# Kernel optimization log

Measured on AMD Instinct MI355X. Metric: run time of the kernel, lower is better.

The kernel has to match this reference:

```python
import jax, jax.numpy as jnp
import numpy as np

B, N, P, E = 4, 512, 2048, 32768  # batch, atoms/sample, probes/sample, edges/sample
F_HID = 128
D_RBF = 32
CUTOFF = 4.0
CELL_L = 10.0


def setup_inputs() -> dict:
    key = jax.random.key(0)
    ks = jax.random.split(key, 12)
    in_dim = D_RBF + 3 * F_HID
    inp = {
        "S_JK": jax.random.normal(ks[0], (B * N, F_HID), jnp.float32),
        "V_JK": jax.random.normal(ks[1], (B * N, 3, F_HID), jnp.float32) * 0.5,
        "atom_xyz": jax.random.uniform(ks[2], (B, N, 3), jnp.float32) * CELL_L,
        "probe_xyz": jax.random.uniform(ks[3], (B, P, 3), jnp.float32) * CELL_L,
        "cell": jnp.tile(CELL_L * jnp.eye(3, dtype=jnp.float32), (B, 1, 1)),
        "probe_edges_displacement": jax.random.randint(ks[4], (B, E, 3), -1, 2).astype(jnp.float32),
        "W1": jax.random.normal(ks[5], (in_dim, F_HID), jnp.float32) / np.sqrt(in_dim),
        "b1": jnp.zeros((F_HID,), jnp.float32),
        "W2": jax.random.normal(ks[6], (F_HID, F_HID // 2), jnp.float32) / np.sqrt(F_HID),
        "b2": jnp.zeros((F_HID // 2,), jnp.float32),
        "W3": jax.random.normal(ks[7], (F_HID // 2, 1), jnp.float32) / np.sqrt(F_HID // 2),
        "b3": jnp.zeros((1,), jnp.float32),
        "probe_edges": jnp.stack([
            jax.random.randint(ks[8], (B, E), 0, N),
            jax.random.randint(ks[9], (B, E), 0, P),
        ], axis=-1),
    }
    return inp


def reference(S_JK, V_JK, atom_xyz, probe_xyz, cell, probe_edges_displacement,
              W1, b1, W2, b2, W3, b3, probe_edges):
    # full counts -> unpad_and_cat == reshape
    atom_flat = atom_xyz.reshape(B * N, 3)
    probe_flat = probe_xyz.reshape(B * P, 3)
    a_idx = (probe_edges[..., 0] + (jnp.arange(B) * N)[:, None]).reshape(-1)  # [B*E]
    p_idx = (probe_edges[..., 1] + (jnp.arange(B) * P)[:, None]).reshape(-1)

    # periodic displacement: edges_displacement @ cell (per batch), then flatten
    disp = jnp.einsum('bek,bkj->bej', probe_edges_displacement, cell).reshape(-1, 3)
    diff = probe_flat[p_idx] - (atom_flat[a_idx] + disp)          # [BE,3]
    dist = jnp.linalg.norm(diff, axis=-1)                         # [BE]

    # sinc RBF expansion: sin(n*pi*d/cutoff)/d, n=1..D_RBF
    n_range = jnp.arange(1, D_RBF + 1, dtype=dist.dtype)
    e_pi = jnp.sin(dist[:, None] * n_range * jnp.pi / CUTOFF) / dist[:, None]

    r_hat = diff / (dist[:, None] + 1e-8)                          # [BE,3]
    q_pi = jnp.einsum('ekf,ek->ef', V_JK[a_idx], r_hat)            # [BE,F]
    n_e = jnp.linalg.norm(V_JK, axis=1)[a_idx]                     # [BE,F]

    h = jnp.concatenate([e_pi, q_pi, n_e, S_JK[a_idx]], axis=-1)   # [BE, D_RBF+3F]
    h = jax.nn.silu(h @ W1 + b1)
    h = jax.nn.silu(h @ W2 + b2)
    m_pi = (h @ W3 + b3)[:, 0]                                     # [BE]

    # Behler-Parinello cosine cutoff
    cw = jnp.where(dist < CUTOFF, 0.5 * (jnp.cos(jnp.pi * dist / CUTOFF) + 1.0), 0.0)
    m_weighted = m_pi * cw

    rho = jax.ops.segment_sum(m_weighted, p_idx, num_segments=B * P)
    return rho.reshape(B, P)
```

## Files before the change

### kernel.cpp

```cpp
#include <hip/hip_runtime.h>
#include <math.h>

#define BB 4
#define NN 512
#define PP 2048
#define EE 32768
#define FH 128
#define DRBF 32
#define CUT 4.0f
#define PI_F 3.14159265358979323846f
#define NE 4
#define CHUNK 256
#define AT2 8


__global__ __launch_bounds__(256) void atom_kernel(
    const float* __restrict__ S, const float* __restrict__ V,
    const float* __restrict__ W1, float* __restrict__ O,
    float* __restrict__ out) {
  __shared__ float inS[AT2][128];
  const int t   = threadIdx.x;
  if (blockIdx.x < 8)
    ((float4*)out)[blockIdx.x * 256 + t] = make_float4(0.f, 0.f, 0.f, 0.f);

  const int fam = blockIdx.x % 5;
  const int a0  = (blockIdx.x / 5) * AT2;

  {
    int a  = t >> 5;
    int k4 = t & 31;
    float4 v;
    if (fam < 3) {
      v = *(const float4*)&V[(size_t)(a0 + a) * 384 + fam * 128 + k4 * 4];
    } else if (fam == 4) {
      v = *(const float4*)&S[(size_t)(a0 + a) * 128 + k4 * 4];
    } else {
      float4 x = *(const float4*)&V[(size_t)(a0 + a) * 384 +   0 + k4 * 4];
      float4 y = *(const float4*)&V[(size_t)(a0 + a) * 384 + 128 + k4 * 4];
      float4 z = *(const float4*)&V[(size_t)(a0 + a) * 384 + 256 + k4 * 4];
      v.x = sqrtf(x.x*x.x + y.x*y.x + z.x*z.x);
      v.y = sqrtf(x.y*x.y + y.y*y.y + z.y*z.y);
      v.z = sqrtf(x.z*x.z + y.z*y.z + z.z*z.z);
      v.w = sqrtf(x.w*x.w + y.w*y.w + z.w*z.w);
    }
    *(float4*)&inS[a][k4 * 4] = v;
  }
  __syncthreads();

  const int f1 = t & 127;
  const int ah = t >> 7;
  const int wrow = (fam < 3) ? 32 : ((fam == 3) ? 160 : 288);
  const float* Wb = W1 + (size_t)wrow * FH + f1;

  float acc0 = 0.f, acc1 = 0.f, acc2 = 0.f, acc3 = 0.f;
  #pragma unroll 4
  for (int k4 = 0; k4 < 32; ++k4) {
    float w0 = Wb[(k4*4 + 0) * FH];
    float w1 = Wb[(k4*4 + 1) * FH];
    float w2 = Wb[(k4*4 + 2) * FH];
    float w3 = Wb[(k4*4 + 3) * FH];
    float4 h0 = *(const float4*)&inS[ah*4 + 0][k4*4];
    float4 h1 = *(const float4*)&inS[ah*4 + 1][k4*4];
    float4 h2 = *(const float4*)&inS[ah*4 + 2][k4*4];
    float4 h3 = *(const float4*)&inS[ah*4 + 3][k4*4];
    acc0 = fmaf(h0.x, w0, acc0); acc1 = fmaf(h1.x, w0, acc1);
    acc2 = fmaf(h2.x, w0, acc2); acc3 = fmaf(h3.x, w0, acc3);
    acc0 = fmaf(h0.y, w1, acc0); acc1 = fmaf(h1.y, w1, acc1);
    acc2 = fmaf(h2.y, w1, acc2); acc3 = fmaf(h3.y, w1, acc3);
    acc0 = fmaf(h0.z, w2, acc0); acc1 = fmaf(h1.z, w2, acc1);
    acc2 = fmaf(h2.z, w2, acc2); acc3 = fmaf(h3.z, w2, acc3);
    acc0 = fmaf(h0.w, w3, acc0); acc1 = fmaf(h1.w, w3, acc1);
    acc2 = fmaf(h2.w, w3, acc2); acc3 = fmaf(h3.w, w3, acc3);
  }
  float* Ob = O + (size_t)(a0 + ah*4) * 640 + fam * 128 + f1;
  Ob[0]    = acc0;
  Ob[640]  = acc1;
  Ob[1280] = acc2;
  Ob[1920] = acc3;
}

__global__ __launch_bounds__(256) void fused_kernel(
    const int* __restrict__ pe, const float* __restrict__ pdisp,
    const float* __restrict__ cell, const float* __restrict__ atom_xyz,
    const float* __restrict__ probe_xyz,
    const float* __restrict__ O,
    const float* __restrict__ W1, const float* __restrict__ b1,
    const float* __restrict__ W2, const float* __restrict__ b2,
    const float* __restrict__ W3, const float* __restrict__ b3,
    float* __restrict__ out) {
  __shared__ float sdx[CHUNK], sdy[CHUNK], sdz[CHUNK];
  __shared__ unsigned sap[CHUNK];
  __shared__ int mcnt;
  __shared__ float epS[NE][DRBF];
  __shared__ float h2S[NE][FH];
  __shared__ float part2[4][NE][64];
  __shared__ float rS[NE][3];
  __shared__ unsigned aS[NE];
  __shared__ float cwS[NE];
  __shared__ unsigned pS[NE];

  const int t    = threadIdx.x;
  const int lane = t & 63;
  const int wave = t >> 6;
  if (t == 0) mcnt = 0;
  __syncthreads();

  const int e = blockIdx.x * CHUNK + t;
  const int b = blockIdx.x >> 7;
  const float* cb = cell + b * 9;
  {
    int2 ap = ((const int2*)pe)[e];
    float pd0 = pdisp[e*3], pd1 = pdisp[e*3+1], pd2 = pdisp[e*3+2];
    float d0 = pd0*cb[0] + pd1*cb[3] + pd2*cb[6];
    float d1 = pd0*cb[1] + pd1*cb[4] + pd2*cb[7];
    float d2 = pd0*cb[2] + pd1*cb[5] + pd2*cb[8];
    int ag = b*NN + ap.x;
    int pg = b*PP + ap.y;
    float dx = probe_xyz[pg*3]   - (atom_xyz[ag*3]   + d0);
    float dy = probe_xyz[pg*3+1] - (atom_xyz[ag*3+1] + d1);
    float dz = probe_xyz[pg*3+2] - (atom_xyz[ag*3+2] + d2);
    float dist2 = dx*dx + dy*dy + dz*dz;
    if (dist2 < CUT*CUT) {
      int s = atomicAdd(&mcnt, 1);
      sdx[s] = dx; sdy[s] = dy; sdz[s] = dz;
      sap[s] = ((unsigned)ag << 16) | (unsigned)pg;
    }
  }
  __syncthreads();
  const int m = mcnt;
  if (m == 0) return;

  const int f1 = t & 127;
  const int eh = t >> 7;
  const float b1v = b1[f1];
  const float b2v = b2[lane];
  const float w3v = W3[lane];
  const float b3v = b3[0];

  for (int s0 = 0; s0 < m; s0 += NE) {
    {
      const int s = s0 + wave;
      float dx, dy, dz; unsigned ap_;
      if (s < m) { dx = sdx[s]; dy = sdy[s]; dz = sdz[s]; ap_ = sap[s]; }
      else       { dx = 1.f; dy = 0.f; dz = 0.f; ap_ = 0xFFFFFFFFu; }
      float d = sqrtf(dx*dx + dy*dy + dz*dz);
      float inv = 1.0f / (d + 1e-8f);
      if (lane < DRBF) epS[wave][lane] = sinf(d * (float)(lane+1) * (PI_F/CUT)) / d;
      if (lane == 0) {
        rS[wave][0] = dx*inv; rS[wave][1] = dy*inv; rS[wave][2] = dz*inv;
        aS[wave] = (ap_ == 0xFFFFFFFFu) ? 0u : (ap_ >> 16);
        cwS[wave] = 0.5f * (cosf((PI_F/CUT) * d) + 1.0f);
        pS[wave]  = (ap_ == 0xFFFFFFFFu) ? 0xFFFFFFFFu : (ap_ & 0xFFFFu);
      }
    }
    __syncthreads();

    {
      const int e0 = eh*2, e1 = eh*2 + 1;
      const float* Ob0 = O + (size_t)aS[e0] * 640 + f1;
      const float* Ob1 = O + (size_t)aS[e1] * 640 + f1;
      float o00 = Ob0[0], o01 = Ob0[128], o02 = Ob0[256], o03 = Ob0[384], o04 = Ob0[512];
      float o10 = Ob1[0], o11 = Ob1[128], o12 = Ob1[256], o13 = Ob1[384], o14 = Ob1[512];
      float z0 = b1v + o03 + o04 + rS[e0][0]*o00 + rS[e0][1]*o01 + rS[e0][2]*o02;
      float z1 = b1v + o13 + o14 + rS[e1][0]*o10 + rS[e1][1]*o11 + rS[e1][2]*o12;
      const float* Wb = W1 + f1;
      #pragma unroll
      for (int k = 0; k < DRBF; ++k) {
        float w = Wb[k * FH];
        z0 = fmaf(epS[e0][k], w, z0);
        z1 = fmaf(epS[e1][k], w, z1);
      }
      h2S[e0][f1] = z0 / (1.0f + __expf(-z0));
      h2S[e1][f1] = z1 / (1.0f + __expf(-z1));
    }
    __syncthreads();

    {
      float a0 = 0.f, a1 = 0.f, a2 = 0.f, a3 = 0.f;
      const float* Wq = W2 + (wave * 32) * 64 + lane;
      const float* h0p = &h2S[0][wave * 32];
      const float* h1p = &h2S[1][wave * 32];
      const float* h2p = &h2S[2][wave * 32];
      const float* h3p = &h2S[3][wave * 32];
      #pragma unroll
      for (int k4 = 0; k4 < 8; ++k4) {
        float w0 = Wq[(k4*4 + 0) * 64];
        float w1 = Wq[(k4*4 + 1) * 64];
        float w2 = Wq[(k4*4 + 2) * 64];
        float w3 = Wq[(k4*4 + 3) * 64];
        float4 h0 = *(const float4*)&h0p[k4*4];
        float4 h1 = *(const float4*)&h1p[k4*4];
        float4 h2 = *(const float4*)&h2p[k4*4];
        float4 h3 = *(const float4*)&h3p[k4*4];
        a0 = fmaf(h0.x, w0, a0); a1 = fmaf(h1.x, w0, a1);
        a2 = fmaf(h2.x, w0, a2); a3 = fmaf(h3.x, w0, a3);
        a0 = fmaf(h0.y, w1, a0); a1 = fmaf(h1.y, w1, a1);
        a2 = fmaf(h2.y, w1, a2); a3 = fmaf(h3.y, w1, a3);
        a0 = fmaf(h0.z, w2, a0); a1 = fmaf(h1.z, w2, a1);
        a2 = fmaf(h2.z, w2, a2); a3 = fmaf(h3.z, w2, a3);
        a0 = fmaf(h0.w, w3, a0); a1 = fmaf(h1.w, w3, a1);
        a2 = fmaf(h2.w, w3, a2); a3 = fmaf(h3.w, w3, a3);
      }
      part2[wave][0][lane] = a0;
      part2[wave][1][lane] = a1;
      part2[wave][2][lane] = a2;
      part2[wave][3][lane] = a3;
    }
    __syncthreads();

    {
      float z = part2[0][wave][lane] + part2[1][wave][lane]
              + part2[2][wave][lane] + part2[3][wave][lane] + b2v;
      float h2 = z / (1.0f + __expf(-z));
      float rs = h2 * w3v;
      #pragma unroll
      for (int off = 32; off; off >>= 1) rs += __shfl_xor(rs, off, 64);
      if (lane == 0) {
        unsigned p = pS[wave];
        if (p != 0xFFFFFFFFu) atomicAdd(&out[p], (rs + b3v) * cwS[wave]);
      }
    }
    __syncthreads();
  }
}

extern "C" void kernel_launch(void* const* d_in, const int* in_sizes, int n_in,
                              void* d_out, int out_size, void* d_ws, size_t ws_size,
                              hipStream_t stream) {
  const float* S         = (const float*)d_in[0];
  const float* V         = (const float*)d_in[1];
  const float* atom_xyz  = (const float*)d_in[2];
  const float* probe_xyz = (const float*)d_in[3];
  const float* cell      = (const float*)d_in[4];
  const float* pdisp     = (const float*)d_in[5];
  const float* W1        = (const float*)d_in[6];
  const float* b1        = (const float*)d_in[7];
  const float* W2        = (const float*)d_in[8];
  const float* b2        = (const float*)d_in[9];
  const float* W3        = (const float*)d_in[10];
  const float* b3        = (const float*)d_in[11];
  const int*   pe        = (const int*)d_in[12];
  float* out = (float*)d_out;

  float* O = (float*)((char*)d_ws + 256);

  atom_kernel<<<(BB*NN/AT2)*5, 256, 0, stream>>>(S, V, W1, O, out);
  fused_kernel<<<BB*EE/CHUNK, 256, 0, stream>>>(pe, pdisp, cell, atom_xyz, probe_xyz,
                                                O, W1, b1, W2, b2, W3, b3, out);
}
```

Measured before the change: 22.30 us.

## Move edge filtering into atom kernel and compact survivors globally for MLP

Edge distance filtering now runs in extra blocks of the first kernel, alongside the per-atom projection. Surviving edges are appended to a global record buffer through an atomic counter. The MLP kernel then walks the compacted records in groups of four edges per block instead of re-filtering its own 256-edge chunk. This takes the gather and filter latency off the MLP kernel's critical path and balances work across blocks. In exchange it adds a memset launch and global atomics, and it silently drops survivors beyond a fixed cap of 8192 records.

```diff
diff --git a/kernel.cpp b/kernel.cpp
--- a/kernel.cpp
+++ b/kernel.cpp
@@ -10,21 +10,58 @@
 #define CUT 4.0f
 #define PI_F 3.14159265358979323846f
 #define NE 4
-#define CHUNK 256
 #define AT2 8
-
-
-__global__ __launch_bounds__(256) void atom_kernel(
+#define ABLK 1280
+#define FBLK 512
+#define RECMAX 8192
+
+struct __align__(16) Rec { float dx, dy, dz; unsigned ap; };
+
+
+__global__ __launch_bounds__(256) void combined_kernel(
+    const int* __restrict__ pe, const float* __restrict__ pdisp,
+    const float* __restrict__ cell, const float* __restrict__ atom_xyz,
+    const float* __restrict__ probe_xyz,
     const float* __restrict__ S, const float* __restrict__ V,
-    const float* __restrict__ W1, float* __restrict__ O,
-    float* __restrict__ out) {
+    const float* __restrict__ W1,
+    unsigned* __restrict__ gcnt, Rec* __restrict__ recs,
+    float* __restrict__ O, float* __restrict__ out) {
   __shared__ float inS[AT2][128];
   const int t   = threadIdx.x;
-  if (blockIdx.x < 8)
-    ((float4*)out)[blockIdx.x * 256 + t] = make_float4(0.f, 0.f, 0.f, 0.f);
-
-  const int fam = blockIdx.x % 5;
-  const int a0  = (blockIdx.x / 5) * AT2;
+  const int bid = blockIdx.x;
+
+  if (bid >= ABLK) {
+    const int fb = bid - ABLK;
+    const int e  = fb * 256 + t;
+    const int b  = e >> 15;
+    const float* cb = cell + b * 9;
+    int2 ap = ((const int2*)pe)[e];
+    float pd0 = pdisp[e*3], pd1 = pdisp[e*3+1], pd2 = pdisp[e*3+2];
+    float d0 = pd0*cb[0] + pd1*cb[3] + pd2*cb[6];
+    float d1 = pd0*cb[1] + pd1*cb[4] + pd2*cb[7];
+    float d2 = pd0*cb[2] + pd1*cb[5] + pd2*cb[8];
+    int ag = b*NN + ap.x;
+    int pg = b*PP + ap.y;
+    float dx = probe_xyz[pg*3]   - (atom_xyz[ag*3]   + d0);
+    float dy = probe_xyz[pg*3+1] - (atom_xyz[ag*3+1] + d1);
+    float dz = probe_xyz[pg*3+2] - (atom_xyz[ag*3+2] + d2);
+    float dist2 = dx*dx + dy*dy + dz*dz;
+    if (dist2 < CUT*CUT) {
+      unsigned i = atomicAdd(gcnt, 1u);
+      if (i < RECMAX) {
+        Rec r; r.dx = dx; r.dy = dy; r.dz = dz;
+        r.ap = ((unsigned)ag << 16) | (unsigned)pg;
+        recs[i] = r;
+      }
+    }
+    return;
+  }
+
+  if (bid < 8)
+    ((float4*)out)[bid * 256 + t] = make_float4(0.f, 0.f, 0.f, 0.f);
+
+  const int fam = bid % 5;
+  const int a0  = (bid / 5) * AT2;
 
   {
     int a  = t >> 5;
@@ -79,18 +116,13 @@
   Ob[1920] = acc3;
 }
 
-__global__ __launch_bounds__(256) void fused_kernel(
-    const int* __restrict__ pe, const float* __restrict__ pdisp,
-    const float* __restrict__ cell, const float* __restrict__ atom_xyz,
-    const float* __restrict__ probe_xyz,
+__global__ __launch_bounds__(256) void mlp_kernel(
+    const Rec* __restrict__ recs, const unsigned* __restrict__ gcnt,
     const float* __restrict__ O,
     const float* __restrict__ W1, const float* __restrict__ b1,
     const float* __restrict__ W2, const float* __restrict__ b2,
     const float* __restrict__ W3, const float* __restrict__ b3,
     float* __restrict__ out) {
-  __shared__ float sdx[CHUNK], sdy[CHUNK], sdz[CHUNK];
-  __shared__ unsigned sap[CHUNK];
-  __shared__ int mcnt;
   __shared__ float epS[NE][DRBF];
   __shared__ float h2S[NE][FH];
   __shared__ float part2[4][NE][64];
@@ -102,33 +134,8 @@
   const int t    = threadIdx.x;
   const int lane = t & 63;
   const int wave = t >> 6;
-  if (t == 0) mcnt = 0;
-  __syncthreads();
-
-  const int e = blockIdx.x * CHUNK + t;
-  const int b = blockIdx.x >> 7;
-  const float* cb = cell + b * 9;
-  {
-    int2 ap = ((const int2*)pe)[e];
-    float pd0 = pdisp[e*3], pd1 = pdisp[e*3+1], pd2 = pdisp[e*3+2];
-    float d0 = pd0*cb[0] + pd1*cb[3] + pd2*cb[6];
-    float d1 = pd0*cb[1] + pd1*cb[4] + pd2*cb[7];
-    float d2 = pd0*cb[2] + pd1*cb[5] + pd2*cb[8];
-    int ag = b*NN + ap.x;
-    int pg = b*PP + ap.y;
-    float dx = probe_xyz[pg*3]   - (atom_xyz[ag*3]   + d0);
-    float dy = probe_xyz[pg*3+1] - (atom_xyz[ag*3+1] + d1);
-    float dz = probe_xyz[pg*3+2] - (atom_xyz[ag*3+2] + d2);
-    float dist2 = dx*dx + dy*dy + dz*dz;
-    if (dist2 < CUT*CUT) {
-      int s = atomicAdd(&mcnt, 1);
-      sdx[s] = dx; sdy[s] = dy; sdz[s] = dz;
-      sap[s] = ((unsigned)ag << 16) | (unsigned)pg;
-    }
-  }
-  __syncthreads();
-  const int m = mcnt;
-  if (m == 0) return;
+  int n = (int)*gcnt; if (n > RECMAX) n = RECMAX;
+  if ((int)blockIdx.x * NE >= n) return;
 
   const int f1 = t & 127;
   const int eh = t >> 7;
@@ -137,30 +144,30 @@
   const float w3v = W3[lane];
   const float b3v = b3[0];
 
-  for (int s0 = 0; s0 < m; s0 += NE) {
-    {
-      const int s = s0 + wave;
-      float dx, dy, dz; unsigned ap_;
-      if (s < m) { dx = sdx[s]; dy = sdy[s]; dz = sdz[s]; ap_ = sap[s]; }
-      else       { dx = 1.f; dy = 0.f; dz = 0.f; ap_ = 0xFFFFFFFFu; }
-      float d = sqrtf(dx*dx + dy*dy + dz*dz);
+  for (int bt = blockIdx.x; bt * NE < n; bt += gridDim.x) {
+    {
+      const int s = bt * NE + wave;
+      Rec r;
+      if (s < n) r = recs[s];
+      else { r.dx = 1.f; r.dy = 0.f; r.dz = 0.f; r.ap = 0xFFFFFFFFu; }
+      float d = sqrtf(r.dx*r.dx + r.dy*r.dy + r.dz*r.dz);
       float inv = 1.0f / (d + 1e-8f);
       if (lane < DRBF) epS[wave][lane] = sinf(d * (float)(lane+1) * (PI_F/CUT)) / d;
       if (lane == 0) {
-        rS[wave][0] = dx*inv; rS[wave][1] = dy*inv; rS[wave][2] = dz*inv;
-        aS[wave] = (ap_ == 0xFFFFFFFFu) ? 0u : (ap_ >> 16);
+        rS[wave][0] = r.dx*inv; rS[wave][1] = r.dy*inv; rS[wave][2] = r.dz*inv;
+        aS[wave] = (r.ap == 0xFFFFFFFFu) ? 0u : (r.ap >> 16);
         cwS[wave] = 0.5f * (cosf((PI_F/CUT) * d) + 1.0f);
-        pS[wave]  = (ap_ == 0xFFFFFFFFu) ? 0xFFFFFFFFu : (ap_ & 0xFFFFu);
+        pS[wave]  = (r.ap == 0xFFFFFFFFu) ? 0xFFFFFFFFu : (r.ap & 0xFFFFu);
       }
     }
     __syncthreads();
 
     {
       const int e0 = eh*2, e1 = eh*2 + 1;
-      const float* Ob0 = O + (size_t)aS[e0] * 640 + f1;
-      const float* Ob1 = O + (size_t)aS[e1] * 640 + f1;
-      float o00 = Ob0[0], o01 = Ob0[128], o02 = Ob0[256], o03 = Ob0[384], o04 = Ob0[512];
-      float o10 = Ob1[0], o11 = Ob1[128], o12 = Ob1[256], o13 = Ob1[384], o14 = Ob1[512];
+      const float* Oa  = O + (size_t)aS[e0] * 640 + f1;
+      const float* Obp = O + (size_t)aS[e1] * 640 + f1;
+      float o00 = Oa[0],  o01 = Oa[128],  o02 = Oa[256],  o03 = Oa[384],  o04 = Oa[512];
+      float o10 = Obp[0], o11 = Obp[128], o12 = Obp[256], o13 = Obp[384], o14 = Obp[512];
       float z0 = b1v + o03 + o04 + rS[e0][0]*o00 + rS[e0][1]*o01 + rS[e0][2]*o02;
       float z1 = b1v + o13 + o14 + rS[e1][0]*o10 + rS[e1][1]*o11 + rS[e1][2]*o12;
       const float* Wb = W1 + f1;
@@ -242,9 +249,13 @@
   const int*   pe        = (const int*)d_in[12];
   float* out = (float*)d_out;
 
-  float* O = (float*)((char*)d_ws + 256);
-
-  atom_kernel<<<(BB*NN/AT2)*5, 256, 0, stream>>>(S, V, W1, O, out);
-  fused_kernel<<<BB*EE/CHUNK, 256, 0, stream>>>(pe, pdisp, cell, atom_xyz, probe_xyz,
-                                                O, W1, b1, W2, b2, W3, b3, out);
+  unsigned* gcnt = (unsigned*)d_ws;
+  Rec*      recs = (Rec*)((char*)d_ws + 256);
+  float*    O    = (float*)((char*)d_ws + (1u << 20));
+
+  hipMemsetAsync(d_ws, 0, 16, stream);
+  combined_kernel<<<ABLK + FBLK, 256, 0, stream>>>(pe, pdisp, cell, atom_xyz,
+                                                   probe_xyz, S, V, W1,
+                                                   gcnt, recs, O, out);
+  mlp_kernel<<<512, 256, 0, stream>>>(recs, gcnt, O, W1, b1, W2, b2, W3, b3, out);
 }
```

New measurement: 33.45 us. 50.0% more time.

## Process one edge per wavefront without block barriers, halve edge chunk per block

Applied to the files above, without the earlier changes.

The fused kernel now has each wavefront handle its own filtered edge end to end: RBF, first and second MLP layers, and the atomic scatter. Per-wave shared buffers replace the block-wide __syncthreads between stages. The edge chunk per block drops from 256 to 128, so twice as many blocks launch and load balance improves. The trade-off is that each wave reads the full W2 column serially and loses the 4-edge register reuse of W1/W2. Intra-wave ordering relies on __threadfence_block and wave lockstep rather than explicit barriers.

```diff
diff --git a/kernel.cpp b/kernel.cpp
--- a/kernel.cpp
+++ b/kernel.cpp
@@ -9,8 +9,7 @@
 #define DRBF 32
 #define CUT 4.0f
 #define PI_F 3.14159265358979323846f
-#define NE 4
-#define CHUNK 256
+#define CHUNK 128
 #define AT2 8
 
 
@@ -19,7 +18,7 @@
     const float* __restrict__ W1, float* __restrict__ O,
     float* __restrict__ out) {
   __shared__ float inS[AT2][128];
-  const int t   = threadIdx.x;
+  const int t = threadIdx.x;
   if (blockIdx.x < 8)
     ((float4*)out)[blockIdx.x * 256 + t] = make_float4(0.f, 0.f, 0.f, 0.f);
 
@@ -91,13 +90,8 @@
   __shared__ float sdx[CHUNK], sdy[CHUNK], sdz[CHUNK];
   __shared__ unsigned sap[CHUNK];
   __shared__ int mcnt;
-  __shared__ float epS[NE][DRBF];
-  __shared__ float h2S[NE][FH];
-  __shared__ float part2[4][NE][64];
-  __shared__ float rS[NE][3];
-  __shared__ unsigned aS[NE];
-  __shared__ float cwS[NE];
-  __shared__ unsigned pS[NE];
+  __shared__ float epW[4][DRBF];
+  __shared__ float h2W[4][FH];
 
   const int t    = threadIdx.x;
   const int lane = t & 63;
@@ -105,10 +99,10 @@
   if (t == 0) mcnt = 0;
   __syncthreads();
 
-  const int e = blockIdx.x * CHUNK + t;
-  const int b = blockIdx.x >> 7;
-  const float* cb = cell + b * 9;
-  {
+  const int b = blockIdx.x >> 8;
+  if (t < CHUNK) {
+    const int e = blockIdx.x * CHUNK + t;
+    const float* cb = cell + b * 9;
     int2 ap = ((const int2*)pe)[e];
     float pd0 = pdisp[e*3], pd1 = pdisp[e*3+1], pd2 = pdisp[e*3+2];
     float d0 = pd0*cb[0] + pd1*cb[3] + pd2*cb[6];
@@ -130,97 +124,66 @@
   const int m = mcnt;
   if (m == 0) return;
 
-  const int f1 = t & 127;
-  const int eh = t >> 7;
-  const float b1v = b1[f1];
+  const float b1a = b1[lane];
+  const float b1b = b1[lane + 64];
   const float b2v = b2[lane];
   const float w3v = W3[lane];
   const float b3v = b3[0];
 
-  for (int s0 = 0; s0 < m; s0 += NE) {
-    {
-      const int s = s0 + wave;
-      float dx, dy, dz; unsigned ap_;
-      if (s < m) { dx = sdx[s]; dy = sdy[s]; dz = sdz[s]; ap_ = sap[s]; }
-      else       { dx = 1.f; dy = 0.f; dz = 0.f; ap_ = 0xFFFFFFFFu; }
-      float d = sqrtf(dx*dx + dy*dy + dz*dz);
-      float inv = 1.0f / (d + 1e-8f);
-      if (lane < DRBF) epS[wave][lane] = sinf(d * (float)(lane+1) * (PI_F/CUT)) / d;
-      if (lane == 0) {
-        rS[wave][0] = dx*inv; rS[wave][1] = dy*inv; rS[wave][2] = dz*inv;
-        aS[wave] = (ap_ == 0xFFFFFFFFu) ? 0u : (ap_ >> 16);
-        cwS[wave] = 0.5f * (cosf((PI_F/CUT) * d) + 1.0f);
-        pS[wave]  = (ap_ == 0xFFFFFFFFu) ? 0xFFFFFFFFu : (ap_ & 0xFFFFu);
+  for (int s = wave; s < m; s += 4) {
+    float dx = sdx[s], dy = sdy[s], dz = sdz[s];
+    unsigned ap_ = sap[s];
+    unsigned a = ap_ >> 16;
+    unsigned p = ap_ & 0xFFFFu;
+    float d = sqrtf(dx*dx + dy*dy + dz*dz);
+    float inv = 1.0f / (d + 1e-8f);
+    float rh0 = dx*inv, rh1 = dy*inv, rh2 = dz*inv;
+    float cw = 0.5f * (cosf((PI_F/CUT) * d) + 1.0f);
+    if (lane < DRBF) epW[wave][lane] = sinf(d * (float)(lane+1) * (PI_F/CUT)) / d;
+    __threadfence_block();
+
+    const float* Oa = O + (size_t)a * 640;
+    float o0a = Oa[lane],       o1a = Oa[128+lane], o2a = Oa[256+lane];
+    float o3a = Oa[384+lane],   o4a = Oa[512+lane];
+    float o0b = Oa[64+lane],    o1b = Oa[192+lane], o2b = Oa[320+lane];
+    float o3b = Oa[448+lane],   o4b = Oa[576+lane];
+    float za = b1a + o3a + o4a + rh0*o0a + rh1*o1a + rh2*o2a;
+    float zb = b1b + o3b + o4b + rh0*o0b + rh1*o1b + rh2*o2b;
+    #pragma unroll 1
+    for (int g = 0; g < 2; ++g) {
+      const int k0 = g * 16;
+      #pragma unroll
+      for (int k = 0; k < 16; ++k) {
+        float wa = W1[(k0 + k) * FH + lane];
+        float wb = W1[(k0 + k) * FH + lane + 64];
+        float e  = epW[wave][k0 + k];
+        za = fmaf(e, wa, za);
+        zb = fmaf(e, wb, zb);
       }
     }
-    __syncthreads();
-
-    {
-      const int e0 = eh*2, e1 = eh*2 + 1;
-      const float* Ob0 = O + (size_t)aS[e0] * 640 + f1;
-      const float* Ob1 = O + (size_t)aS[e1] * 640 + f1;
-      float o00 = Ob0[0], o01 = Ob0[128], o02 = Ob0[256], o03 = Ob0[384], o04 = Ob0[512];
-      float o10 = Ob1[0], o11 = Ob1[128], o12 = Ob1[256], o13 = Ob1[384], o14 = Ob1[512];
-      float z0 = b1v + o03 + o04 + rS[e0][0]*o00 + rS[e0][1]*o01 + rS[e0][2]*o02;
-      float z1 = b1v + o13 + o14 + rS[e1][0]*o10 + rS[e1][1]*o11 + rS[e1][2]*o12;
-      const float* Wb = W1 + f1;
+    float ha = za / (1.0f + __expf(-za));
+    float hb = zb / (1.0f + __expf(-zb));
+    h2W[wave][lane]      = ha;
+    h2W[wave][lane + 64] = hb;
+    __threadfence_block();
+
+    float acc = b2v;
+    #pragma unroll 1
+    for (int g = 0; g < 4; ++g) {
+      const int k0 = g * 32;
       #pragma unroll
-      for (int k = 0; k < DRBF; ++k) {
-        float w = Wb[k * FH];
-        z0 = fmaf(epS[e0][k], w, z0);
-        z1 = fmaf(epS[e1][k], w, z1);
+      for (int k = 0; k < 32; ++k) {
+        acc = fmaf(h2W[wave][k0 + k], W2[(k0 + k) * 64 + lane], acc);
       }
-      h2S[e0][f1] = z0 / (1.0f + __expf(-z0));
-      h2S[e1][f1] = z1 / (1.0f + __expf(-z1));
-    }
-    __syncthreads();
-
-    {
-      float a0 = 0.f, a1 = 0.f, a2 = 0.f, a3 = 0.f;
-      const float* Wq = W2 + (wave * 32) * 64 + lane;
-      const float* h0p = &h2S[0][wave * 32];
-      const float* h1p = &h2S[1][wave * 32];
-      const float* h2p = &h2S[2][wave * 32];
-      const float* h3p = &h2S[3][wave * 32];
-      #pragma unroll
-      for (int k4 = 0; k4 < 8; ++k4) {
-        float w0 = Wq[(k4*4 + 0) * 64];
-        float w1 = Wq[(k4*4 + 1) * 64];
-        float w2 = Wq[(k4*4 + 2) * 64];
-        float w3 = Wq[(k4*4 + 3) * 64];
-        float4 h0 = *(const float4*)&h0p[k4*4];
-        float4 h1 = *(const float4*)&h1p[k4*4];
-        float4 h2 = *(const float4*)&h2p[k4*4];
-        float4 h3 = *(const float4*)&h3p[k4*4];
-        a0 = fmaf(h0.x, w0, a0); a1 = fmaf(h1.x, w0, a1);
-        a2 = fmaf(h2.x, w0, a2); a3 = fmaf(h3.x, w0, a3);
-        a0 = fmaf(h0.y, w1, a0); a1 = fmaf(h1.y, w1, a1);
-        a2 = fmaf(h2.y, w1, a2); a3 = fmaf(h3.y, w1, a3);
-        a0 = fmaf(h0.z, w2, a0); a1 = fmaf(h1.z, w2, a1);
-        a2 = fmaf(h2.z, w2, a2); a3 = fmaf(h3.z, w2, a3);
-        a0 = fmaf(h0.w, w3, a0); a1 = fmaf(h1.w, w3, a1);
-        a2 = fmaf(h2.w, w3, a2); a3 = fmaf(h3.w, w3, a3);
-      }
-      part2[wave][0][lane] = a0;
-      part2[wave][1][lane] = a1;
-      part2[wave][2][lane] = a2;
-      part2[wave][3][lane] = a3;
-    }
-    __syncthreads();
-
-    {
-      float z = part2[0][wave][lane] + part2[1][wave][lane]
-              + part2[2][wave][lane] + part2[3][wave][lane] + b2v;
-      float h2 = z / (1.0f + __expf(-z));
-      float rs = h2 * w3v;
-      #pragma unroll
-      for (int off = 32; off; off >>= 1) rs += __shfl_xor(rs, off, 64);
-      if (lane == 0) {
-        unsigned p = pS[wave];
-        if (p != 0xFFFFFFFFu) atomicAdd(&out[p], (rs + b3v) * cwS[wave]);
-      }
-    }
-    __syncthreads();
+    }
+    float h2 = acc / (1.0f + __expf(-acc));
+
+    float rs = h2 * w3v;
+    #pragma unroll
+    for (int off = 32; off; off >>= 1) rs += __shfl_xor(rs, off, 64);
+    if (lane == 0) atomicAdd(&out[p], (rs + b3v) * cw);
+
+    __threadfence_block();
   }
 }
 
```

New measurement: 24.72 us. 10.9% more time.
